# Optimization experiments

Hardware: AMD Instinct MI355X
Metric: run time of the kernel (lower is better)

Reference implementation:

```python
import jax, jax.numpy as jnp
import numpy as np

MEM_SIZE = 2048
CELL = 64
R_HEADS = 4
IN_SIZE = 512
IFACE = CELL * R_HEADS + CELL + 2 * CELL + 2 * R_HEADS + 5  # 461
DELTA = 1e-6
EPS = 1e-6


def setup_inputs() -> dict:
    key = jax.random.key(0)
    ks = jax.random.split(key, 8)
    b = 256
    return {
        'xi': jax.random.normal(ks[0], (b, IN_SIZE), jnp.float32),
        'W': jax.random.normal(ks[1], (IFACE, IN_SIZE), jnp.float32) * 0.05,
        'gamma': jnp.ones((IFACE,), jnp.float32),
        'beta': jnp.zeros((IFACE,), jnp.float32),
        'memory': jax.random.normal(ks[2], (b, MEM_SIZE, CELL), jnp.float32),
        'read_weights': jax.random.uniform(ks[3], (b, R_HEADS, MEM_SIZE), jnp.float32),
        'write_weights': jax.random.uniform(ks[4], (b, 1, MEM_SIZE), jnp.float32),
        'usage': jax.random.uniform(ks[5], (b, MEM_SIZE), jnp.float32),
    }


def _cosine(mem, keys):
    # mem: (b,m,c), keys: (b,k,c) -> (b,k,m)
    mem_n = mem / (jnp.linalg.norm(mem, axis=-1, keepdims=True) + EPS)
    key_n = keys / (jnp.linalg.norm(keys, axis=-1, keepdims=True) + EPS)
    return jnp.einsum('bkc,bmc->bkm', key_n, mem_n)


def reference(xi, W, gamma, beta, memory, read_weights, write_weights, usage):
    b = xi.shape[0]
    r, k, w, m = R_HEADS, CELL, CELL, MEM_SIZE

    # interface projection + GroupNorm(1, C) over channel dim
    itf = xi @ W.T
    mu = jnp.mean(itf, axis=1, keepdims=True)
    var = jnp.var(itf, axis=1, keepdims=True)
    itf = (itf - mu) / jnp.sqrt(var + 1e-5) * gamma + beta

    c = 0
    read_keys = jnp.tanh(itf[:, c:c + r * k].reshape(b, r, k)); c += r * k
    read_strengths = jax.nn.softplus(itf[:, c:c + r]); c += r
    write_key = jnp.tanh(itf[:, c:c + k].reshape(b, 1, k)); c += k
    write_strength = jax.nn.softplus(itf[:, c]).reshape(b, 1); c += 1
    erase_vec = jax.nn.sigmoid(itf[:, c:c + w].reshape(b, 1, w)); c += w
    write_vec = jnp.tanh(itf[:, c:c + w].reshape(b, 1, w)); c += w
    free_gates = jax.nn.sigmoid(itf[:, c:c + r]); c += r
    alloc_gate = jax.nn.softmax(itf[:, c:c + 3], axis=1); c += 3
    write_gate = jax.nn.sigmoid(itf[:, c]).reshape(b, 1)

    # ---- usage update ----
    u = usage + (1 - usage) * (1 - jnp.prod(1 - write_weights, axis=1))
    psi = jnp.prod(1 - free_gates[:, :, None] * read_weights, axis=1)  # (b,m)
    u = u * psi

    # ---- content weighting for write ----
    wcw = jax.nn.softmax(_cosine(memory, write_key) * write_strength[:, :, None], axis=2)  # (b,1,m)

    # ---- allocation ----
    u2 = DELTA + (1 - DELTA) * u
    idx = jnp.argsort(u2, axis=1)                              # ascending usage (phi)
    su = jnp.take_along_axis(u2, idx, axis=1)                  # sorted usage
    cp = jnp.cumprod(jnp.concatenate([jnp.ones((b, 1), u2.dtype), su], axis=1), axis=1)[:, :-1]
    sa = (1 - su) * cp
    inv = jnp.argsort(idx, axis=1)                             # inverse permutation (phi_rev)
    alloc = jnp.take_along_axis(sa, inv, axis=1)               # (b,m)

    # ---- write weighting ----
    fw = (alloc_gate[:, 0:1] * jnp.mean(read_weights, axis=1)
          + alloc_gate[:, 1:2] * alloc
          + alloc_gate[:, 2:3] * wcw[:, 0])
    ww = (write_gate * fw)[:, None, :]                         # (b,1,m)

    # ---- memory write (erase + add) ----
    reset_gate = jnp.prod(1 - ww[:, :, :, None] * erase_vec[:, :, None, :], axis=1)  # (b,m,w)
    mem = memory * reset_gate + jnp.einsum('bm,bw->bmw', ww[:, 0], write_vec[:, 0])

    # ---- read ----
    rw = jax.nn.softmax(_cosine(mem, read_keys) * read_strengths[:, :, None], axis=2)  # (b,r,m)
    read_vectors = jnp.einsum('brm,bmw->brw', rw, mem)         # (b,r,w)
    return read_vectors
```

## Files before the change

kernel.cpp:

```cpp
#include <hip/hip_runtime.h>
#include <math.h>

#define MM    2048
#define CC    64
#define RH    4
#define NIF   461
#define INS   512
#define EPSN  1e-6f

typedef unsigned long long u64;

#define OFF_P    ((size_t)0)
#define OFF_U2   ((size_t)131072)
#define OFF_MRW  ((size_t)655360)
#define OFF_SC   ((size_t)1179648)
#define OFF_WW   ((size_t)1703936)
#define OFF_PART ((size_t)2228224)

__global__ __launch_bounds__(512) void k1_interface(
    const float* __restrict__ xi, const float* __restrict__ W,
    const float* __restrict__ gamma, const float* __restrict__ beta,
    const float* __restrict__ read_w, const float* __restrict__ write_w,
    const float* __restrict__ usage, float* __restrict__ ws)
{
  const int b = blockIdx.x, tid = threadIdx.x;
  const int lane = tid & 63, wid = tid >> 6;
  __shared__ __align__(16) float s_xi[512], s_itf[512], s_act[512];
  __shared__ float sRed[24];

  s_xi[tid] = xi[(size_t)b*INS + tid];
  __syncthreads();

  {
    const float4 x0 = ((const float4*)s_xi)[lane*2];
    const float4 x1 = ((const float4*)s_xi)[lane*2+1];
    for (int col = wid; col < NIF; col += 8) {
      const float4* Wr = (const float4*)(W + (size_t)col*INS);
      float4 a0 = Wr[lane*2], a1 = Wr[lane*2+1];
      float p = a0.x*x0.x + a0.y*x0.y + a0.z*x0.z + a0.w*x0.w
              + a1.x*x1.x + a1.y*x1.y + a1.z*x1.z + a1.w*x1.w;
      #pragma unroll
      for (int off=1; off<64; off<<=1) p += __shfl_xor(p, off);
      if (lane==0) s_itf[col] = p;
    }
  }
  __syncthreads();

  {
    float v = (tid < NIF) ? s_itf[tid] : 0.f;
    float s = v, q = v*v;
    #pragma unroll
    for (int off=1; off<64; off<<=1) { s += __shfl_xor(s,off); q += __shfl_xor(q,off); }
    if (lane==0){ sRed[wid] = s; sRed[8+wid] = q; }
    __syncthreads();
    if (tid==0){
      float ts=0.f, tq=0.f;
      for (int i=0;i<8;i++){ ts+=sRed[i]; tq+=sRed[8+i]; }
      float mean = ts/(float)NIF;
      float var  = tq/(float)NIF - mean*mean;
      sRed[16]=mean; sRed[17]=rsqrtf(var+1e-5f);
    }
    __syncthreads();
    float mean = sRed[16], rstd = sRed[17];
    if (tid < NIF) {
      float g = (s_itf[tid]-mean)*rstd*gamma[tid] + beta[tid];
      float a;
      if      (tid < 256) a = tanhf(g);
      else if (tid < 260) a = fmaxf(g,0.f) + log1pf(expf(-fabsf(g)));
      else if (tid < 324) a = tanhf(g);
      else if (tid ==324) a = fmaxf(g,0.f) + log1pf(expf(-fabsf(g)));
      else if (tid < 389) a = 1.f/(1.f+expf(-g));
      else if (tid < 453) a = tanhf(g);
      else if (tid < 457) a = 1.f/(1.f+expf(-g));
      else if (tid < 460) a = g;
      else                a = 1.f/(1.f+expf(-g));
      s_act[tid] = a;
    }
  }
  __syncthreads();

  float* P = ws + OFF_P + (size_t)b*512;
  if (wid < 4) {
    float t = s_act[wid*64 + lane];
    float q = t*t;
    #pragma unroll
    for (int off=1; off<64; off<<=1) q += __shfl_xor(q,off);
    P[wid*64+lane] = t * (s_act[256+wid] / (sqrtf(q) + EPSN));
  } else if (wid == 4) {
    float t = s_act[260+lane];
    float q = t*t;
    #pragma unroll
    for (int off=1; off<64; off<<=1) q += __shfl_xor(q,off);
    P[256+lane] = t * (s_act[324] / (sqrtf(q) + EPSN));
  } else if (wid == 5) {
    P[320+lane] = s_act[325+lane];
    P[384+lane] = s_act[389+lane];
  } else if (wid == 6 && lane == 0) {
    float a0=s_act[457], a1=s_act[458], a2=s_act[459];
    float mx = fmaxf(a0, fmaxf(a1,a2));
    float e0=expf(a0-mx), e1=expf(a1-mx), e2=expf(a2-mx);
    float is = 1.f/(e0+e1+e2);
    P[448]=e0*is; P[449]=e1*is; P[450]=e2*is; P[451]=s_act[460];
  }

  {
    const float4* us4 = (const float4*)(usage   + (size_t)b*MM);
    const float4* wr4 = (const float4*)(write_w + (size_t)b*MM);
    const float4* rw4 = (const float4*)(read_w  + (size_t)b*RH*MM);
    const float fg0=s_act[453], fg1=s_act[454], fg2=s_act[455], fg3=s_act[456];
    float4 u = us4[tid], w = wr4[tid];
    float4 r0 = rw4[tid], r1 = rw4[512+tid], r2 = rw4[1024+tid], r3 = rw4[1536+tid];
    float4 mr, u2o;
    mr.x = 0.25f*(r0.x+r1.x+r2.x+r3.x);
    mr.y = 0.25f*(r0.y+r1.y+r2.y+r3.y);
    mr.z = 0.25f*(r0.z+r1.z+r2.z+r3.z);
    mr.w = 0.25f*(r0.w+r1.w+r2.w+r3.w);
    #define U2C(comp)                                                           \
    { float uu  = u.comp + (1.f-u.comp)*w.comp;                                 \
      float psi = (1.f-fg0*r0.comp)*(1.f-fg1*r1.comp)*(1.f-fg2*r2.comp)*(1.f-fg3*r3.comp); \
      u2o.comp = 1e-6f + (1.f-1e-6f)*(uu*psi); }
    U2C(x) U2C(y) U2C(z) U2C(w)
    #undef U2C
    ((float4*)(ws + OFF_MRW + (size_t)b*MM))[tid] = mr;
    ((float4*)(ws + OFF_U2  + (size_t)b*MM))[tid] = u2o;
  }
}

__global__ __launch_bounds__(256) void k2_scores(
    const float* __restrict__ memory, float* __restrict__ ws)
{
  const int slice = blockIdx.x, b = blockIdx.y;
  const int tid = threadIdx.x, l16 = tid & 15, rowg = tid >> 4;
  const float* P = ws + OFF_P + (size_t)b*512;
  const float4 wk4 = ((const float4*)(P+256))[l16];
  const float4* mem4 = (const float4*)(memory + (size_t)b*MM*CC) + (size_t)slice*256*16;
  float* sc = ws + OFF_SC + (size_t)b*MM + slice*256;
  #pragma unroll 4
  for (int it = 0; it < 16; ++it) {
    int m = it*16 + rowg;
    float4 v = mem4[m*16 + l16];
    float d = v.x*wk4.x + v.y*wk4.y + v.z*wk4.z + v.w*wk4.w;
    float q = v.x*v.x + v.y*v.y + v.z*v.z + v.w*v.w;
    #pragma unroll
    for (int off=1; off<16; off<<=1){ d += __shfl_xor(d,off); q += __shfl_xor(q,off); }
    if (l16==0) sc[m] = d / (sqrtf(q)+EPSN);
  }
}

__global__ __launch_bounds__(1024) void k3_sortww(float* __restrict__ ws)
{
  const int b = blockIdx.x, tid = threadIdx.x;
  const int lane = tid & 63, wid = tid >> 6;
  __shared__ __align__(16) u64   sKeys[2048];
  __shared__ __align__(16) float sA[2048], sB[2048];
  __shared__ float sRed[20];

  const float* u2p = ws + OFF_U2 + (size_t)b*MM;
  for (int i = tid; i < MM; i += 1024)
    sKeys[i] = ((u64)__float_as_uint(u2p[i])<<32) | (unsigned)i;

  for (int k = 2; k <= MM; k <<= 1) {
    for (int j = k >> 1; j > 0; j >>= 1) {
      __syncthreads();
      for (int i = tid; i < MM; i += 1024) {
        int ixj = i ^ j;
        if (ixj > i) {
          u64 a = sKeys[i], c = sKeys[ixj];
          bool up = ((i & k) == 0);
          if ((a > c) == up) { sKeys[i] = c; sKeys[ixj] = a; }
        }
      }
    }
  }
  __syncthreads();

  for (int i = tid; i < MM; i += 1024)
    sA[i] = __uint_as_float((unsigned)(sKeys[i]>>32));
  __syncthreads();
  float* src = sA; float* dst = sB;
  for (int d = 1; d < MM; d <<= 1) {
    for (int i = tid; i < MM; i += 1024) {
      float v = src[i];
      if (i >= d) v *= src[i-d];
      dst[i] = v;
    }
    __syncthreads();
    float* t = src; src = dst; dst = t;
  }
  for (int i = tid; i < MM; i += 1024) {
    u64 kk = sKeys[i];
    float su  = __uint_as_float((unsigned)(kk>>32));
    unsigned idx = (unsigned)(kk & 0xFFFFFFFFu);
    float cp = (i>0) ? src[i-1] : 1.f;
    dst[idx] = (1.f - su)*cp;
  }
  __syncthreads();
  float* allocBuf = dst;

  float* sF = (float*)sKeys;
  const float* scp = ws + OFF_SC + (size_t)b*MM;
  float lm = -INFINITY;
  for (int i = tid; i < MM; i += 1024) { float v = scp[i]; sF[i] = v; lm = fmaxf(lm, v); }
  #pragma unroll
  for (int off=1; off<64; off<<=1) lm = fmaxf(lm, __shfl_xor(lm,off));
  if (lane==0) sRed[wid] = lm;
  __syncthreads();
  if (tid==0){ float mx=sRed[0]; for(int i=1;i<16;i++) mx=fmaxf(mx,sRed[i]); sRed[16]=mx; }
  __syncthreads();
  float mx = sRed[16];
  float ls = 0.f;
  for (int i = tid; i < MM; i += 1024) { float e = expf(sF[i]-mx); sF[i]=e; ls += e; }
  #pragma unroll
  for (int off=1; off<64; off<<=1) ls += __shfl_xor(ls,off);
  if (lane==0) sRed[wid] = ls;
  __syncthreads();
  if (tid==0){ float s=0.f; for(int i=0;i<16;i++) s+=sRed[i]; sRed[17]=1.f/s; }
  __syncthreads();
  float inv = sRed[17];

  const float* P = ws + OFF_P + (size_t)b*512;
  const float ag0=P[448], ag1=P[449], ag2=P[450], wg=P[451];
  const float* mrwp = ws + OFF_MRW + (size_t)b*MM;
  float* wwp = ws + OFF_WW + (size_t)b*MM;
  for (int i = tid; i < MM; i += 1024)
    wwp[i] = wg*(ag0*mrwp[i] + ag1*allocBuf[i] + ag2*sF[i]*inv);
}

__global__ __launch_bounds__(256) void k4_passB(
    const float* __restrict__ memory, float* __restrict__ ws)
{
  const int slice = blockIdx.x, b = blockIdx.y;
  const int tid = threadIdx.x, l16 = tid & 15, rowg = tid >> 4;
  const int lane = tid & 63, wid = tid >> 6;
  __shared__ __align__(16) float chunk[64*68];
  __shared__ __align__(16) float sE[4*68];
  __shared__ float sHm[4], sHs[4], sHsc[4];

  const float* P = ws + OFF_P + (size_t)b*512;
  const float4 er4 = ((const float4*)(P+320))[l16];
  const float4 wv4 = ((const float4*)(P+384))[l16];
  const float4 k0 = ((const float4*)P)[     l16];
  const float4 k1 = ((const float4*)P)[16 + l16];
  const float4 k2 = ((const float4*)P)[32 + l16];
  const float4 k3 = ((const float4*)P)[48 + l16];
  const float* wwp = ws + OFF_WW + (size_t)b*MM + slice*256;
  const float4* mem4 = (const float4*)(memory + (size_t)b*MM*CC) + (size_t)slice*256*16;

  if (tid < 4){ sHm[tid] = -INFINITY; sHs[tid] = 0.f; }
  __syncthreads();
  float acc = 0.f;

  for (int ch = 0; ch < 4; ++ch) {
    #pragma unroll
    for (int pp = 0; pp < 4; ++pp) {
      int p = pp*16 + rowg;
      int m = ch*64 + p;
      float4 v = mem4[m*16 + l16];
      float wm = wwp[m];
      float4 nv;
      nv.x = v.x*(1.f - wm*er4.x) + wm*wv4.x;
      nv.y = v.y*(1.f - wm*er4.y) + wm*wv4.y;
      nv.z = v.z*(1.f - wm*er4.z) + wm*wv4.z;
      nv.w = v.w*(1.f - wm*er4.w) + wm*wv4.w;
      *(float4*)&chunk[p*68 + (l16<<2)] = nv;
      float d0 = nv.x*k0.x+nv.y*k0.y+nv.z*k0.z+nv.w*k0.w;
      float d1 = nv.x*k1.x+nv.y*k1.y+nv.z*k1.z+nv.w*k1.w;
      float d2 = nv.x*k2.x+nv.y*k2.y+nv.z*k2.z+nv.w*k2.w;
      float d3 = nv.x*k3.x+nv.y*k3.y+nv.z*k3.z+nv.w*k3.w;
      float q  = nv.x*nv.x+nv.y*nv.y+nv.z*nv.z+nv.w*nv.w;
      #pragma unroll
      for (int off=1; off<16; off<<=1){
        d0+=__shfl_xor(d0,off); d1+=__shfl_xor(d1,off);
        d2+=__shfl_xor(d2,off); d3+=__shfl_xor(d3,off);
        q +=__shfl_xor(q ,off);
      }
      if (l16==0){
        float inv = 1.f/(sqrtf(q)+EPSN);
        sE[      p] = d0*inv;
        sE[ 68 + p] = d1*inv;
        sE[136 + p] = d2*inv;
        sE[204 + p] = d3*inv;
      }
    }
    __syncthreads();
    {
      float v = sE[wid*68 + lane];
      float cm = v;
      #pragma unroll
      for (int off=1; off<64; off<<=1) cm = fmaxf(cm, __shfl_xor(cm,off));
      float om = sHm[wid];
      float nm = fmaxf(om, cm);
      float scl = expf(om - nm);
      float e = expf(v - nm);
      sE[wid*68 + lane] = e;
      float es = e;
      #pragma unroll
      for (int off=1; off<64; off<<=1) es += __shfl_xor(es,off);
      if (lane==0){
        sHs[wid] = sHs[wid]*scl + es;
        sHm[wid] = nm;
        sHsc[wid] = scl;
      }
    }
    __syncthreads();
    {
      float scl = sHsc[wid];
      acc *= scl;
      #pragma unroll 8
      for (int p = 0; p < 64; ++p)
        acc += sE[wid*68 + p] * chunk[p*68 + lane];
    }
    __syncthreads();
  }

  float* part = ws + OFF_PART + ((size_t)(b*8 + slice))*264;
  part[wid*66 + 2 + lane] = acc;
  if (lane==0){ part[wid*66 + 0] = sHm[wid]; part[wid*66 + 1] = sHs[wid]; }
}

__global__ __launch_bounds__(256) void k5_combine(
    const float* __restrict__ ws, float* __restrict__ out)
{
  const int b = blockIdx.x, tid = threadIdx.x;
  const int head = tid >> 6, c = tid & 63;
  const float* part = ws + OFF_PART + (size_t)b*8*264;
  float M = -INFINITY;
  #pragma unroll
  for (int s = 0; s < 8; ++s) M = fmaxf(M, part[s*264 + head*66]);
  float S = 0.f, A = 0.f;
  #pragma unroll
  for (int s = 0; s < 8; ++s) {
    float w = expf(part[s*264 + head*66] - M);
    S += w * part[s*264 + head*66 + 1];
    A += w * part[s*264 + head*66 + 2 + c];
  }
  out[((size_t)b<<8) + head*64 + c] = A / S;
}

extern "C" void kernel_launch(void* const* d_in, const int* in_sizes, int n_in,
                              void* d_out, int out_size, void* d_ws, size_t ws_size,
                              hipStream_t stream) {
  const float* xi      = (const float*)d_in[0];
  const float* W       = (const float*)d_in[1];
  const float* gamma   = (const float*)d_in[2];
  const float* beta    = (const float*)d_in[3];
  const float* memory  = (const float*)d_in[4];
  const float* read_w  = (const float*)d_in[5];
  const float* write_w = (const float*)d_in[6];
  const float* usage   = (const float*)d_in[7];
  float* ws  = (float*)d_ws;
  float* out = (float*)d_out;

  k1_interface<<<dim3(256), dim3(512), 0, stream>>>(xi, W, gamma, beta, read_w, write_w, usage, ws);
  k2_scores  <<<dim3(8,256), dim3(256), 0, stream>>>(memory, ws);
  k3_sortww  <<<dim3(256), dim3(1024), 0, stream>>>(ws);
  k4_passB   <<<dim3(8,256), dim3(256), 0, stream>>>(memory, ws);
  k5_combine <<<dim3(256), dim3(256), 0, stream>>>(ws, out);
}
```

Baseline: 152.0 us.

## Run sort concurrently with score pass, rework scan and readout accumulation

The bitonic sort and allocation computation now run in 256 extra blocks of the same launch as the write-key score pass, so the sort overlaps the memory-bound scoring. The sort drops from 1024 to 256 threads, uses index arithmetic so no lanes sit idle, and the Hillis-Steele product scan is replaced by a per-thread serial scan plus a wave shuffle scan. The softmax and write-weight step becomes a small vectorised kernel. In passB each lane accumulates a float4 over a quarter of the rows, followed by a cross-lane reduction, which uses wider LDS reads. The partial results are split into separate accumulator and statistics buffers. The risk is that a 256-thread sort block runs longer and could become the tail of the fused launch.

```diff
diff --git a/kernel.cpp b/kernel.cpp
--- a/kernel.cpp
+++ b/kernel.cpp
@@ -10,12 +10,14 @@
 
 typedef unsigned long long u64;
 
-#define OFF_P    ((size_t)0)
-#define OFF_U2   ((size_t)131072)
-#define OFF_MRW  ((size_t)655360)
-#define OFF_SC   ((size_t)1179648)
-#define OFF_WW   ((size_t)1703936)
-#define OFF_PART ((size_t)2228224)
+#define OFF_P     ((size_t)0)
+#define OFF_U2    ((size_t)131072)
+#define OFF_MRW   ((size_t)655360)
+#define OFF_SC    ((size_t)1179648)
+#define OFF_ALLOC ((size_t)1703936)
+#define OFF_WW    ((size_t)2228224)
+#define OFF_PART  ((size_t)2752512)
+#define OFF_PSTAT ((size_t)3276800)
 
 __global__ __launch_bounds__(512) void k1_interface(
     const float* __restrict__ xi, const float* __restrict__ W,
@@ -126,104 +128,131 @@
   }
 }
 
-__global__ __launch_bounds__(256) void k2_scores(
+__global__ __launch_bounds__(256) void k2_fused(
     const float* __restrict__ memory, float* __restrict__ ws)
 {
-  const int slice = blockIdx.x, b = blockIdx.y;
-  const int tid = threadIdx.x, l16 = tid & 15, rowg = tid >> 4;
-  const float* P = ws + OFF_P + (size_t)b*512;
-  const float4 wk4 = ((const float4*)(P+256))[l16];
-  const float4* mem4 = (const float4*)(memory + (size_t)b*MM*CC) + (size_t)slice*256*16;
-  float* sc = ws + OFF_SC + (size_t)b*MM + slice*256;
-  #pragma unroll 4
-  for (int it = 0; it < 16; ++it) {
-    int m = it*16 + rowg;
-    float4 v = mem4[m*16 + l16];
-    float d = v.x*wk4.x + v.y*wk4.y + v.z*wk4.z + v.w*wk4.w;
-    float q = v.x*v.x + v.y*v.y + v.z*v.z + v.w*v.w;
-    #pragma unroll
-    for (int off=1; off<16; off<<=1){ d += __shfl_xor(d,off); q += __shfl_xor(q,off); }
-    if (l16==0) sc[m] = d / (sqrtf(q)+EPSN);
-  }
-}
-
-__global__ __launch_bounds__(1024) void k3_sortww(float* __restrict__ ws)
+  __shared__ __align__(16) u64 sKeys[2048];
+  __shared__ float sT[260];
+  const int tid = threadIdx.x;
+
+  if (blockIdx.x < 256) {
+    const int b = blockIdx.x;
+    const int lane = tid & 63, w = tid >> 6;
+    const float* u2p = ws + OFF_U2 + (size_t)b*MM;
+    for (int i = tid; i < MM; i += 256)
+      sKeys[i] = ((u64)__float_as_uint(u2p[i])<<32) | (unsigned)i;
+    __syncthreads();
+
+    for (int k = 2; k <= MM; k <<= 1) {
+      for (int j = k >> 1; j > 0; j >>= 1) {
+        #pragma unroll 4
+        for (int c = tid; c < MM/2; c += 256) {
+          int i   = ((c & ~(j-1)) << 1) | (c & (j-1));
+          int ixj = i | j;
+          u64 a = sKeys[i], d = sKeys[ixj];
+          bool up = ((i & k) == 0);
+          if ((a > d) == up) { sKeys[i] = d; sKeys[ixj] = a; }
+        }
+        __syncthreads();
+      }
+    }
+
+    float p[8];
+    {
+      float run = 1.f;
+      #pragma unroll
+      for (int e = 0; e < 8; ++e) {
+        float su = __uint_as_float((unsigned)(sKeys[tid*8+e]>>32));
+        run *= su; p[e] = run;
+      }
+      sT[tid] = run;
+    }
+    __syncthreads();
+    float v = sT[tid];
+    float incl = v;
+    #pragma unroll
+    for (int off=1; off<64; off<<=1) {
+      float n = __shfl_up(incl, off);
+      if (lane >= off) incl *= n;
+    }
+    float excl = __shfl_up(incl, 1);
+    if (lane == 0) excl = 1.f;
+    if (lane == 63) sT[256 + w] = incl;
+    __syncthreads();
+    float base = 1.f;
+    for (int ww2 = 0; ww2 < w; ++ww2) base *= sT[256 + ww2];
+    float E = base * excl;
+
+    float* allocp = ws + OFF_ALLOC + (size_t)b*MM;
+    #pragma unroll
+    for (int e = 0; e < 8; ++e) {
+      u64 kk = sKeys[tid*8+e];
+      float su = __uint_as_float((unsigned)(kk>>32));
+      unsigned idx = (unsigned)(kk & 0xFFFFFFFFu);
+      float cp = E * (e ? p[e-1] : 1.f);
+      allocp[idx] = (1.f - su) * cp;
+    }
+  } else {
+    const int f = blockIdx.x - 256;
+    const int b = f >> 3, slice = f & 7;
+    const int l16 = tid & 15, rowg = tid >> 4;
+    const float* P = ws + OFF_P + (size_t)b*512;
+    const float4 wk4 = ((const float4*)(P+256))[l16];
+    const float4* mem4 = (const float4*)(memory + (size_t)b*MM*CC) + (size_t)slice*256*16;
+    float* sc = ws + OFF_SC + (size_t)b*MM + slice*256;
+    #pragma unroll 4
+    for (int it = 0; it < 16; ++it) {
+      int m = it*16 + rowg;
+      float4 vv = mem4[m*16 + l16];
+      float d = vv.x*wk4.x + vv.y*wk4.y + vv.z*wk4.z + vv.w*wk4.w;
+      float q = vv.x*vv.x + vv.y*vv.y + vv.z*vv.z + vv.w*vv.w;
+      #pragma unroll
+      for (int off=1; off<16; off<<=1){ d += __shfl_xor(d,off); q += __shfl_xor(q,off); }
+      if (l16==0) sc[m] = d / (sqrtf(q)+EPSN);
+    }
+  }
+}
+
+__global__ __launch_bounds__(256) void k3_ww(float* __restrict__ ws)
 {
   const int b = blockIdx.x, tid = threadIdx.x;
-  const int lane = tid & 63, wid = tid >> 6;
-  __shared__ __align__(16) u64   sKeys[2048];
-  __shared__ __align__(16) float sA[2048], sB[2048];
-  __shared__ float sRed[20];
-
-  const float* u2p = ws + OFF_U2 + (size_t)b*MM;
-  for (int i = tid; i < MM; i += 1024)
-    sKeys[i] = ((u64)__float_as_uint(u2p[i])<<32) | (unsigned)i;
-
-  for (int k = 2; k <= MM; k <<= 1) {
-    for (int j = k >> 1; j > 0; j >>= 1) {
-      __syncthreads();
-      for (int i = tid; i < MM; i += 1024) {
-        int ixj = i ^ j;
-        if (ixj > i) {
-          u64 a = sKeys[i], c = sKeys[ixj];
-          bool up = ((i & k) == 0);
-          if ((a > c) == up) { sKeys[i] = c; sKeys[ixj] = a; }
-        }
-      }
-    }
-  }
-  __syncthreads();
-
-  for (int i = tid; i < MM; i += 1024)
-    sA[i] = __uint_as_float((unsigned)(sKeys[i]>>32));
-  __syncthreads();
-  float* src = sA; float* dst = sB;
-  for (int d = 1; d < MM; d <<= 1) {
-    for (int i = tid; i < MM; i += 1024) {
-      float v = src[i];
-      if (i >= d) v *= src[i-d];
-      dst[i] = v;
-    }
-    __syncthreads();
-    float* t = src; src = dst; dst = t;
-  }
-  for (int i = tid; i < MM; i += 1024) {
-    u64 kk = sKeys[i];
-    float su  = __uint_as_float((unsigned)(kk>>32));
-    unsigned idx = (unsigned)(kk & 0xFFFFFFFFu);
-    float cp = (i>0) ? src[i-1] : 1.f;
-    dst[idx] = (1.f - su)*cp;
-  }
-  __syncthreads();
-  float* allocBuf = dst;
-
-  float* sF = (float*)sKeys;
-  const float* scp = ws + OFF_SC + (size_t)b*MM;
-  float lm = -INFINITY;
-  for (int i = tid; i < MM; i += 1024) { float v = scp[i]; sF[i] = v; lm = fmaxf(lm, v); }
+  const int lane = tid & 63, w = tid >> 6;
+  __shared__ float sR[8];
+  const float4* sc4 = (const float4*)(ws + OFF_SC + (size_t)b*MM);
+  float4 v0 = sc4[tid*2], v1 = sc4[tid*2+1];
+  float m = fmaxf(fmaxf(fmaxf(v0.x,v0.y),fmaxf(v0.z,v0.w)),
+                  fmaxf(fmaxf(v1.x,v1.y),fmaxf(v1.z,v1.w)));
   #pragma unroll
-  for (int off=1; off<64; off<<=1) lm = fmaxf(lm, __shfl_xor(lm,off));
-  if (lane==0) sRed[wid] = lm;
-  __syncthreads();
-  if (tid==0){ float mx=sRed[0]; for(int i=1;i<16;i++) mx=fmaxf(mx,sRed[i]); sRed[16]=mx; }
-  __syncthreads();
-  float mx = sRed[16];
-  float ls = 0.f;
-  for (int i = tid; i < MM; i += 1024) { float e = expf(sF[i]-mx); sF[i]=e; ls += e; }
+  for (int off=1; off<64; off<<=1) m = fmaxf(m, __shfl_xor(m,off));
+  if (lane==0) sR[w] = m;
+  __syncthreads();
+  m = fmaxf(fmaxf(sR[0],sR[1]), fmaxf(sR[2],sR[3]));
+  float e0=expf(v0.x-m), e1=expf(v0.y-m), e2=expf(v0.z-m), e3=expf(v0.w-m);
+  float e4=expf(v1.x-m), e5=expf(v1.y-m), e6=expf(v1.z-m), e7=expf(v1.w-m);
+  float s = e0+e1+e2+e3+e4+e5+e6+e7;
   #pragma unroll
-  for (int off=1; off<64; off<<=1) ls += __shfl_xor(ls,off);
-  if (lane==0) sRed[wid] = ls;
-  __syncthreads();
-  if (tid==0){ float s=0.f; for(int i=0;i<16;i++) s+=sRed[i]; sRed[17]=1.f/s; }
-  __syncthreads();
-  float inv = sRed[17];
+  for (int off=1; off<64; off<<=1) s += __shfl_xor(s,off);
+  if (lane==0) sR[4+w] = s;
+  __syncthreads();
+  float inv = 1.f/(sR[4]+sR[5]+sR[6]+sR[7]);
 
   const float* P = ws + OFF_P + (size_t)b*512;
   const float ag0=P[448], ag1=P[449], ag2=P[450], wg=P[451];
-  const float* mrwp = ws + OFF_MRW + (size_t)b*MM;
-  float* wwp = ws + OFF_WW + (size_t)b*MM;
-  for (int i = tid; i < MM; i += 1024)
-    wwp[i] = wg*(ag0*mrwp[i] + ag1*allocBuf[i] + ag2*sF[i]*inv);
+  const float4* mr4 = (const float4*)(ws + OFF_MRW   + (size_t)b*MM);
+  const float4* al4 = (const float4*)(ws + OFF_ALLOC + (size_t)b*MM);
+  float4* ww4 = (float4*)(ws + OFF_WW + (size_t)b*MM);
+  float4 mra = mr4[tid*2], mrb = mr4[tid*2+1];
+  float4 ala = al4[tid*2], alb = al4[tid*2+1];
+  float4 oa, ob;
+  oa.x = wg*(ag0*mra.x + ag1*ala.x + ag2*e0*inv);
+  oa.y = wg*(ag0*mra.y + ag1*ala.y + ag2*e1*inv);
+  oa.z = wg*(ag0*mra.z + ag1*ala.z + ag2*e2*inv);
+  oa.w = wg*(ag0*mra.w + ag1*ala.w + ag2*e3*inv);
+  ob.x = wg*(ag0*mrb.x + ag1*alb.x + ag2*e4*inv);
+  ob.y = wg*(ag0*mrb.y + ag1*alb.y + ag2*e5*inv);
+  ob.z = wg*(ag0*mrb.z + ag1*alb.z + ag2*e6*inv);
+  ob.w = wg*(ag0*mrb.w + ag1*alb.w + ag2*e7*inv);
+  ww4[tid*2] = oa; ww4[tid*2+1] = ob;
 }
 
 __global__ __launch_bounds__(256) void k4_passB(
@@ -248,7 +277,8 @@
 
   if (tid < 4){ sHm[tid] = -INFINITY; sHs[tid] = 0.f; }
   __syncthreads();
-  float acc = 0.f;
+  const int q = lane & 15, ps = lane >> 4;
+  float4 acc; acc.x=acc.y=acc.z=acc.w=0.f;
 
   for (int ch = 0; ch < 4; ++ch) {
     #pragma unroll
@@ -267,15 +297,15 @@
       float d1 = nv.x*k1.x+nv.y*k1.y+nv.z*k1.z+nv.w*k1.w;
       float d2 = nv.x*k2.x+nv.y*k2.y+nv.z*k2.z+nv.w*k2.w;
       float d3 = nv.x*k3.x+nv.y*k3.y+nv.z*k3.z+nv.w*k3.w;
-      float q  = nv.x*nv.x+nv.y*nv.y+nv.z*nv.z+nv.w*nv.w;
+      float qq = nv.x*nv.x+nv.y*nv.y+nv.z*nv.z+nv.w*nv.w;
       #pragma unroll
       for (int off=1; off<16; off<<=1){
         d0+=__shfl_xor(d0,off); d1+=__shfl_xor(d1,off);
         d2+=__shfl_xor(d2,off); d3+=__shfl_xor(d3,off);
-        q +=__shfl_xor(q ,off);
+        qq+=__shfl_xor(qq,off);
       }
       if (l16==0){
-        float inv = 1.f/(sqrtf(q)+EPSN);
+        float inv = 1.f/(sqrtf(qq)+EPSN);
         sE[      p] = d0*inv;
         sE[ 68 + p] = d1*inv;
         sE[136 + p] = d2*inv;
@@ -305,17 +335,33 @@
     __syncthreads();
     {
       float scl = sHsc[wid];
-      acc *= scl;
-      #pragma unroll 8
-      for (int p = 0; p < 64; ++p)
-        acc += sE[wid*68 + p] * chunk[p*68 + lane];
-    }
-    __syncthreads();
-  }
-
-  float* part = ws + OFF_PART + ((size_t)(b*8 + slice))*264;
-  part[wid*66 + 2 + lane] = acc;
-  if (lane==0){ part[wid*66 + 0] = sHm[wid]; part[wid*66 + 1] = sHs[wid]; }
+      acc.x*=scl; acc.y*=scl; acc.z*=scl; acc.w*=scl;
+      #pragma unroll
+      for (int pp = 0; pp < 16; ++pp) {
+        int p = ps*16 + pp;
+        float e = sE[wid*68 + p];
+        const float4 mv = *(const float4*)&chunk[p*68 + (q<<2)];
+        acc.x += e*mv.x; acc.y += e*mv.y; acc.z += e*mv.z; acc.w += e*mv.w;
+      }
+    }
+    __syncthreads();
+  }
+
+  #pragma unroll
+  for (int off=16; off<64; off<<=1) {
+    acc.x += __shfl_xor(acc.x, off);
+    acc.y += __shfl_xor(acc.y, off);
+    acc.z += __shfl_xor(acc.z, off);
+    acc.w += __shfl_xor(acc.w, off);
+  }
+  if (ps == 0) {
+    float* pacc = ws + OFF_PART + ((((size_t)b*8 + slice)*4 + wid)<<6);
+    *(float4*)&pacc[q<<2] = acc;
+  }
+  if (lane == 0) {
+    float* pst = ws + OFF_PSTAT + (((size_t)b*8 + slice)*4 + wid)*2;
+    pst[0] = sHm[wid]; pst[1] = sHs[wid];
+  }
 }
 
 __global__ __launch_bounds__(256) void k5_combine(
@@ -323,16 +369,17 @@
 {
   const int b = blockIdx.x, tid = threadIdx.x;
   const int head = tid >> 6, c = tid & 63;
-  const float* part = ws + OFF_PART + (size_t)b*8*264;
   float M = -INFINITY;
   #pragma unroll
-  for (int s = 0; s < 8; ++s) M = fmaxf(M, part[s*264 + head*66]);
+  for (int s = 0; s < 8; ++s)
+    M = fmaxf(M, ws[OFF_PSTAT + (((size_t)b*8 + s)*4 + head)*2]);
   float S = 0.f, A = 0.f;
   #pragma unroll
   for (int s = 0; s < 8; ++s) {
-    float w = expf(part[s*264 + head*66] - M);
-    S += w * part[s*264 + head*66 + 1];
-    A += w * part[s*264 + head*66 + 2 + c];
+    const float* pst = ws + OFF_PSTAT + (((size_t)b*8 + s)*4 + head)*2;
+    float w = expf(pst[0] - M);
+    S += w * pst[1];
+    A += w * ws[OFF_PART + ((((size_t)b*8 + s)*4 + head)<<6) + c];
   }
   out[((size_t)b<<8) + head*64 + c] = A / S;
 }
@@ -352,8 +399,8 @@
   float* out = (float*)d_out;
 
   k1_interface<<<dim3(256), dim3(512), 0, stream>>>(xi, W, gamma, beta, read_w, write_w, usage, ws);
-  k2_scores  <<<dim3(8,256), dim3(256), 0, stream>>>(memory, ws);
-  k3_sortww  <<<dim3(256), dim3(1024), 0, stream>>>(ws);
+  k2_fused   <<<dim3(2304), dim3(256), 0, stream>>>(memory, ws);
+  k3_ww      <<<dim3(256), dim3(256), 0, stream>>>(ws);
   k4_passB   <<<dim3(8,256), dim3(256), 0, stream>>>(memory, ws);
   k5_combine <<<dim3(256), dim3(256), 0, stream>>>(ws, out);
 }
```

New measurement: 132.3 us. 1.15x faster.
